# Optimization experiments

Measured on AMD Instinct MI355X. Metric: run time of the kernel, lower is better.

The kernel has to match this reference:

```python
import jax, jax.numpy as jnp
import numpy as np

N_NODES = 50000
N_EDGES = 800000
D = 128


def setup_inputs() -> dict:
    key = jax.random.key(0)
    ks = jax.random.split(key, 8)
    s = 1.0 / np.sqrt(D)
    return {
        "x": jax.random.normal(ks[0], (N_NODES, D), dtype=jnp.float32),
        "edge_index": jax.random.randint(ks[1], (2, N_EDGES), 0, N_NODES, dtype=jnp.int32),
        "W0l": jax.random.normal(ks[2], (D, D), dtype=jnp.float32) * s,
        "b0l": jnp.zeros((D,), dtype=jnp.float32),
        "W0r": jax.random.normal(ks[3], (D, D), dtype=jnp.float32) * s,
        "W1l": jax.random.normal(ks[4], (D, D), dtype=jnp.float32) * s,
        "b1l": jnp.zeros((D,), dtype=jnp.float32),
        "W1r": jax.random.normal(ks[5], (D, D), dtype=jnp.float32) * s,
    }


def reference(x, edge_index, W0l, b0l, W0r, W1l, b1l, W1r):
    # Encoder(conv='sage', num_layers=2), eval mode (dropout = identity).
    src = edge_index[0]  # x_j gathered from source nodes
    dst = edge_index[1]  # aggregated at target nodes
    # in-degree for mean aggregation; isolated nodes get 0 aggregate (PyG mean)
    deg = jax.ops.segment_sum(jnp.ones_like(dst, dtype=x.dtype), dst, num_segments=N_NODES)
    inv_deg = jnp.where(deg > 0, 1.0 / jnp.maximum(deg, 1.0), 0.0)[:, None]

    def sage(h, Wl, bl, Wr):
        m = h @ Wl + bl                                        # lin_l
        agg = jax.ops.segment_sum(m[src], dst, num_segments=N_NODES) * inv_deg  # mean aggr
        return agg + h @ Wr                                    # + lin_r skip

    h = jax.nn.relu(sage(x, W0l, b0l, W0r))   # layer 0 + relu
    return sage(h, W1l, b1l, W1r)             # final layer
```

## Files before the change

kernel.cpp:

```cpp
#include <hip/hip_runtime.h>

#define N_NODES 50000
#define N_EDGES 800000
#define D 128
#define CAP64 64
#define EIDXN (N_NODES * CAP64)

#define NSB 196
#define EPB 4096
#define NFB 1563
#define CCAP 20
#define SEDGE_CAP 768

typedef __bf16 bf16x8 __attribute__((ext_vector_type(8)));
typedef short s16x8 __attribute__((ext_vector_type(8)));
typedef float f32x4 __attribute__((ext_vector_type(4)));
typedef float f32x2 __attribute__((ext_vector_type(2)));
typedef unsigned short u16;
typedef unsigned int u32;
typedef unsigned char u8;
typedef u32 u32x2 __attribute__((ext_vector_type(2)));
typedef u32 u32x4 __attribute__((ext_vector_type(4)));
typedef u16 u16x4 __attribute__((ext_vector_type(4)));

__device__ inline u16 f32_to_bf16(float f) {
    u32 u = __builtin_bit_cast(u32, f);
    u += 0x7fffu + ((u >> 16) & 1u);
    return (u16)(u >> 16);
}

__device__ inline f32x4 mfma16(s16x8 a, s16x8 b, f32x4 c) {
    return __builtin_amdgcn_mfma_f32_16x16x32_bf16(
        __builtin_bit_cast(bf16x8, a), __builtin_bit_cast(bf16x8, b), c, 0, 0, 0);
}

#define CAST_BLOCKS ((N_NODES * 16) / 256)

__global__ __launch_bounds__(256) void prep_stage(
    const float* __restrict__ x, u16* __restrict__ xb,
    u8* __restrict__ xf8, u8* __restrict__ hf8,
    const float* __restrict__ W0l, const float* __restrict__ W0r,
    const float* __restrict__ W1l, const float* __restrict__ W1r,
    u16* __restrict__ Wp,
    const int* __restrict__ src, const int* __restrict__ dst,
    u32* __restrict__ staged, u8* __restrict__ ccnt) {
    __shared__ u32 cnt[NFB];
    int t = threadIdx.x, b = blockIdx.x;
    if (b < CAST_BLOCKS) {
        int gid = b * 256 + t;
        const float* p = x + (size_t)gid * 8;
        f32x4 a = *(const f32x4*)p;
        f32x4 c = *(const f32x4*)(p + 4);
        u16 o[8];
#pragma unroll
        for (int j = 0; j < 4; j++) { o[j] = f32_to_bf16(a[j]); o[4 + j] = f32_to_bf16(c[j]); }
        *(s16x8*)(xb + (size_t)gid * 8) = *(const s16x8*)o;
        int p0 = __builtin_amdgcn_cvt_pk_fp8_f32(a.x, a.y, 0, false);
        int p1 = __builtin_amdgcn_cvt_pk_fp8_f32(a.z, a.w, 0, false);
        int p2 = __builtin_amdgcn_cvt_pk_fp8_f32(c.x, c.y, 0, false);
        int p3 = __builtin_amdgcn_cvt_pk_fp8_f32(c.z, c.w, 0, false);
        u32x2 w;
        w.x = (u32)(p0 & 0xffff) | ((u32)(p1 & 0xffff) << 16);
        w.y = (u32)(p2 & 0xffff) | ((u32)(p3 & 0xffff) << 16);
        *(u32x2*)(xf8 + (size_t)gid * 8) = w;
    } else if (b < CAST_BLOCKS + 32) {
        int gid = (b - CAST_BLOCKS) * 256 + t;
        int wsel = gid >> 11;
        int rem  = gid & 2047;
        int ct   = rem >> 8;
        int ks   = (rem >> 6) & 3;
        int lane = rem & 63;
        const float* W = (wsel == 0) ? W0l : (wsel == 1) ? W0r : (wsel == 2) ? W1l : W1r;
        int n  = ct * 16 + (lane & 15);
        int k0 = ks * 32 + (lane >> 4) * 8;
        u16 o[8];
#pragma unroll
        for (int j = 0; j < 8; j++) o[j] = f32_to_bf16(W[(k0 + j) * D + n]);
        u16* dp = Wp + wsel * 16384 + (size_t)((ct * 4 + ks) * 64 + lane) * 8;
        *(s16x8*)dp = *(const s16x8*)o;
    } else if (b < CAST_BLOCKS + 33) {
        if (t < 32)       ((u32*)(xf8 + (size_t)N_NODES * D))[t] = 0;
        else if (t < 64)  ((u32*)(hf8 + (size_t)N_NODES * D))[t - 32] = 0;
    } else {
        int sb = b - CAST_BLOCKS - 33;
        for (int i = t; i < NFB; i += 256) cnt[i] = 0;
        __syncthreads();
        int bb = sb * EPB;
#pragma unroll
        for (int i = 0; i < 16; i++) {
            int e = bb + i * 256 + t;
            if (e < N_EDGES) {
                int sv = src[e], dv = dst[e];
                int fb = dv >> 5;
                u32 slot = atomicAdd(&cnt[fb], 1);
                if (slot < CCAP)
                    staged[((size_t)sb * NFB + fb) * CCAP + slot] =
                        (u32)sv | ((u32)(dv & 31) << 16);
            }
        }
        __syncthreads();
        for (int i = t; i < NFB; i += 256) {
            u32 c = cnt[i]; if (c > CCAP) c = CCAP;
            ccnt[(size_t)i * NSB + sb] = (u8)c;
        }
    }
}

__global__ __launch_bounds__(256) void fine_kernel(
    const u32* __restrict__ staged, const u8* __restrict__ ccnt,
    u16* __restrict__ eidx, int* __restrict__ cursor) {
    __shared__ u32 sedge[SEDGE_CAP];
    __shared__ u32 ncnt[32];
    __shared__ u32 total;
    int t = threadIdx.x, fb = blockIdx.x;
    if (t < 32) ncnt[t] = 0;
    if (t == 0) total = 0;
    __syncthreads();
    if (t < NSB) {
        u32 c = ccnt[(size_t)fb * NSB + t];
        if (c) {
            u32 base = atomicAdd(&total, c);
            const u32* sp = staged + ((size_t)t * NFB + fb) * CCAP;
            for (u32 j = 0; j < c; j++) {
                u32 bj = base + j;
                if (bj < SEDGE_CAP) sedge[bj] = sp[j];
            }
        }
    }
    __syncthreads();
    u32 tot = total; if (tot > SEDGE_CAP) tot = SEDGE_CAP;
    for (u32 i = t; i < tot; i += 256) {
        u32 v = sedge[i];
        u32 n32 = (v >> 16) & 31;
        u32 slot = atomicAdd(&ncnt[n32], 1);
        int node = (fb << 5) + (int)n32;
        if (slot < CAP64) eidx[((size_t)node << 6) + slot] = (u16)(v & 0xffffu);
    }
    __syncthreads();
    int node = (fb << 5) + t;
    if (t < 32 && node < N_NODES) {
        u32 dgc = ncnt[t]; if (dgc > CAP64) dgc = CAP64;
        cursor[node] = (int)dgc;
    }
}

__device__ inline void issue_e(u16x4 (&e)[2], const u16* __restrict__ eidx,
                               const int (&basek)[2], const int (&rnds)[2],
                               int quad, int rr) {
#pragma unroll
    for (int k = 0; k < 2; k++)
        if (rr < rnds[k]) e[k] = *(const u16x4*)(eidx + basek[k] + rr * 16 + quad * 4);
}
__device__ inline void issue_g(u32x2 (&g)[2][4], const u16x4 (&e)[2],
                               const u8* __restrict__ AF8, const int (&rnds)[2],
                               const int (&degk)[2], int quad, int ql, int rr) {
#pragma unroll
    for (int k = 0; k < 2; k++)
        if (rr < rnds[k]) {
            int sbase = rr * 16 + quad * 4;
#pragma unroll
            for (int j = 0; j < 4; j++) {
                int idx = (sbase + j < degk[k]) ? (int)e[k][j] : N_NODES;
                g[k][j] = *(const u32x2*)(AF8 + (size_t)idx * D + ql * 8);
            }
        }
}
__device__ inline void unpack_acc(f32x2 (&acc)[2][4], const u32x2 (&g)[2][4],
                                  const int (&rnds)[2], int rr) {
#pragma unroll
    for (int k = 0; k < 2; k++)
        if (rr < rnds[k]) {
#pragma unroll
            for (int j = 0; j < 4; j++) {
                u32x2 v = g[k][j];
                acc[k][0] += __builtin_amdgcn_cvt_pk_f32_fp8((int)v.x, false);
                acc[k][1] += __builtin_amdgcn_cvt_pk_f32_fp8((int)v.x, true);
                acc[k][2] += __builtin_amdgcn_cvt_pk_f32_fp8((int)v.y, false);
                acc[k][3] += __builtin_amdgcn_cvt_pk_f32_fp8((int)v.y, true);
            }
        }
}

template <int RELU, int OUTF32>
__global__ __launch_bounds__(512) void fused_layer(
    const u16* __restrict__ A, const u8* __restrict__ AF8,
    const u16* __restrict__ WpR, const u16* __restrict__ WpL,
    const float* __restrict__ bias, const int* __restrict__ cursor,
    const u16* __restrict__ eidx,
    u16* __restrict__ outb, u8* __restrict__ outf8, float* __restrict__ outf) {
    __shared__ char mlds[16 * 256];
    int wave = threadIdx.x >> 6, lane = threadIdx.x & 63;
    int rowbase = blockIdx.x * 16;
    int quad = lane >> 4, ql = lane & 15;

    int basek[2], rnds[2], degk[2];
#pragma unroll
    for (int k = 0; k < 2; k++) {
        int node = rowbase + wave * 2 + k;
        int dd = cursor[node];
        if (dd > CAP64) dd = CAP64;
        degk[k]  = dd;
        basek[k] = node << 6;
        rnds[k]  = (dd + 15) >> 4;
    }
    int maxr = rnds[0] > rnds[1] ? rnds[0] : rnds[1];

    f32x2 acc[2][4];
#pragma unroll
    for (int k = 0; k < 2; k++)
#pragma unroll
        for (int e = 0; e < 4; e++) acc[k][e] = (f32x2){0.f, 0.f};

    if (maxr > 0) {
        u16x4 eA[2], eB[2];
        u32x2 gA[2][4], gB[2][4];
        issue_e(eA, eidx, basek, rnds, quad, 0);
        issue_g(gA, eA, AF8, rnds, degk, quad, ql, 0);
        if (maxr > 1) issue_e(eB, eidx, basek, rnds, quad, 1);
        int r = 0;
        while (true) {
            if (r + 1 < maxr) issue_g(gB, eB, AF8, rnds, degk, quad, ql, r + 1);
            if (r + 2 < maxr) issue_e(eA, eidx, basek, rnds, quad, r + 2);
            unpack_acc(acc, gA, rnds, r);
            if (++r >= maxr) break;
            if (r + 1 < maxr) issue_g(gA, eA, AF8, rnds, degk, quad, ql, r + 1);
            if (r + 2 < maxr) issue_e(eB, eidx, basek, rnds, quad, r + 2);
            unpack_acc(acc, gB, rnds, r);
            if (++r >= maxr) break;
        }
    }

#pragma unroll
    for (int k = 0; k < 2; k++) {
        float v[8];
#pragma unroll
        for (int e = 0; e < 4; e++) { v[2 * e] = acc[k][e].x; v[2 * e + 1] = acc[k][e].y; }
#pragma unroll
        for (int j = 0; j < 8; j++) {
            v[j] += __shfl_xor(v[j], 16);
            v[j] += __shfl_xor(v[j], 32);
        }
        if (quad == 0) {
            float iv = degk[k] > 0 ? 1.0f / (float)degk[k] : 0.0f;
            u32x4 o;
            o.x = (u32)f32_to_bf16(v[0] * iv) | ((u32)f32_to_bf16(v[1] * iv) << 16);
            o.y = (u32)f32_to_bf16(v[2] * iv) | ((u32)f32_to_bf16(v[3] * iv) << 16);
            o.z = (u32)f32_to_bf16(v[4] * iv) | ((u32)f32_to_bf16(v[5] * iv) << 16);
            o.w = (u32)f32_to_bf16(v[6] * iv) | ((u32)f32_to_bf16(v[7] * iv) << 16);
            int lr = wave * 2 + k;
            *(u32x4*)(mlds + lr * 256 + ((ql ^ lr) & 15) * 16) = o;
        }
    }

    s16x8 bR[4], bL[4];
#pragma unroll
    for (int ks = 0; ks < 4; ks++) {
        size_t off = (size_t)((wave * 4 + ks) * 64 + lane) * 8;
        bR[ks] = *(const s16x8*)(WpR + off);
        bL[ks] = *(const s16x8*)(WpL + off);
    }
    __syncthreads();

    f32x4 acc2 = (f32x4){0.f, 0.f, 0.f, 0.f};
#pragma unroll
    for (int ks = 0; ks < 4; ks++) {
        s16x8 a1 = *(const s16x8*)(A + (size_t)(rowbase + ql) * D + ks * 32 + quad * 8);
        s16x8 a2 = *(const s16x8*)(mlds + ql * 256 + (((ks * 4 + quad) ^ ql) & 15) * 16);
        acc2 = mfma16(a1, bR[ks], acc2);
        acc2 = mfma16(a2, bL[ks], acc2);
    }

    float bv = bias[wave * 16 + ql];

#pragma unroll
    for (int i = 0; i < 4; i++) {
        int row = rowbase + quad * 4 + i;
        float mask = cursor[row] > 0 ? 1.f : 0.f;
        int col = wave * 16 + ql;
        float val = acc2[i] + mask * bv;
        if (RELU) val = val > 0.f ? val : 0.f;
        if (OUTF32) {
            outf[(size_t)row * D + col] = val;
        } else {
            outb[(size_t)row * D + col] = f32_to_bf16(val);
            int pk = __builtin_amdgcn_cvt_pk_fp8_f32(val, val, 0, false);
            outf8[(size_t)row * D + col] = (u8)(pk & 0xff);
        }
    }
}

extern "C" void kernel_launch(void* const* d_in, const int* in_sizes, int n_in,
                              void* d_out, int out_size, void* d_ws, size_t ws_size,
                              hipStream_t stream) {
    const float* x    = (const float*)d_in[0];
    const int*   edge = (const int*)d_in[1];
    const int*   src  = edge;
    const int*   dstn = edge + N_EDGES;
    const float* W0l  = (const float*)d_in[2];
    const float* b0l  = (const float*)d_in[3];
    const float* W0r  = (const float*)d_in[4];
    const float* W1l  = (const float*)d_in[5];
    const float* b1l  = (const float*)d_in[6];
    const float* W1r  = (const float*)d_in[7];
    float* out = (float*)d_out;

    char* p = (char*)d_ws;
    auto alloc = [&](size_t nb) { char* r = p; p += (nb + 255) & ~(size_t)255; return r; };
    int*   cursor = (int*)alloc((size_t)N_NODES * 4);
    u16*   eidx   = (u16*)alloc((size_t)EIDXN * 2);
    u16*   xb     = (u16*)alloc((size_t)N_NODES * D * 2);
    u16*   hb     = (u16*)alloc((size_t)N_NODES * D * 2);
    u8*    xf8    = (u8*)alloc((size_t)(N_NODES + 1) * D);
    u8*    hf8    = (u8*)alloc((size_t)(N_NODES + 1) * D);
    u16*   Wp     = (u16*)alloc((size_t)4 * 16384 * 2);
    u32*   staged = (u32*)alloc((size_t)NSB * NFB * CCAP * 4);
    u8*    ccnt   = (u8*)alloc((size_t)NFB * NSB);

    prep_stage<<<CAST_BLOCKS + 33 + NSB, 256, 0, stream>>>(
        x, xb, xf8, hf8, W0l, W0r, W1l, W1r, Wp, src, dstn, staged, ccnt);
    fine_kernel<<<NFB, 256, 0, stream>>>(staged, ccnt, eidx, cursor);

    int fblocks = N_NODES / 16;
    const u16* WpL0 = Wp;
    const u16* WpR0 = Wp + 16384;
    const u16* WpL1 = Wp + 2 * 16384;
    const u16* WpR1 = Wp + 3 * 16384;
    fused_layer<1, 0><<<fblocks, 512, 0, stream>>>(xb, xf8, WpR0, WpL0, b0l, cursor, eidx, hb, hf8, nullptr);
    fused_layer<0, 1><<<fblocks, 512, 0, stream>>>(hb, hf8, WpR1, WpL1, b1l, cursor, eidx, nullptr, nullptr, out);
}
```

Before: 210.1 us.

## Fuse prep, bucketing and both SAGE layers into one cooperative persistent kernel

Replaces the four launches (prep, fine bucketing, two fused layers) with a single cooperative kernel that uses grid.sync between phases. Bucketing now groups destinations by 16 instead of 32, matching the 16-row layer tile. The fine bucketing step and the layer-0 tile run in the same block, so layer 0 reads edge indices and degrees from LDS rather than global memory. The aim is to remove launch gaps and the eidx/cursor round trip for layer 0. In exchange the grid is capped by occupancy, so blocks loop over tiles, the grid barriers add cost, and the smaller per-bucket caps (CCAP 14, SEDGE_CAP 384) may drop edges for high-degree destination groups.

```diff
diff --git a/kernel.cpp b/kernel.cpp
--- a/kernel.cpp
+++ b/kernel.cpp
@@ -1,16 +1,21 @@
 #include <hip/hip_runtime.h>
+#include <hip/hip_cooperative_groups.h>
+
+namespace cg = cooperative_groups;
 
 #define N_NODES 50000
 #define N_EDGES 800000
 #define D 128
 #define CAP64 64
-#define EIDXN (N_NODES * CAP64)
-
+#define NBUCK 3125
 #define NSB 196
 #define EPB 4096
-#define NFB 1563
-#define CCAP 20
-#define SEDGE_CAP 768
+#define CCAP 14
+#define SEDGE_CAP 384
+
+#define CAST_UNITS 1563
+#define WU 16
+#define A_UNITS (CAST_UNITS + WU + 1 + NSB)
 
 typedef __bf16 bf16x8 __attribute__((ext_vector_type(8)));
 typedef short s16x8 __attribute__((ext_vector_type(8)));
@@ -34,126 +39,16 @@
         __builtin_bit_cast(bf16x8, a), __builtin_bit_cast(bf16x8, b), c, 0, 0, 0);
 }
 
-#define CAST_BLOCKS ((N_NODES * 16) / 256)
-
-__global__ __launch_bounds__(256) void prep_stage(
-    const float* __restrict__ x, u16* __restrict__ xb,
-    u8* __restrict__ xf8, u8* __restrict__ hf8,
-    const float* __restrict__ W0l, const float* __restrict__ W0r,
-    const float* __restrict__ W1l, const float* __restrict__ W1r,
-    u16* __restrict__ Wp,
-    const int* __restrict__ src, const int* __restrict__ dst,
-    u32* __restrict__ staged, u8* __restrict__ ccnt) {
-    __shared__ u32 cnt[NFB];
-    int t = threadIdx.x, b = blockIdx.x;
-    if (b < CAST_BLOCKS) {
-        int gid = b * 256 + t;
-        const float* p = x + (size_t)gid * 8;
-        f32x4 a = *(const f32x4*)p;
-        f32x4 c = *(const f32x4*)(p + 4);
-        u16 o[8];
-#pragma unroll
-        for (int j = 0; j < 4; j++) { o[j] = f32_to_bf16(a[j]); o[4 + j] = f32_to_bf16(c[j]); }
-        *(s16x8*)(xb + (size_t)gid * 8) = *(const s16x8*)o;
-        int p0 = __builtin_amdgcn_cvt_pk_fp8_f32(a.x, a.y, 0, false);
-        int p1 = __builtin_amdgcn_cvt_pk_fp8_f32(a.z, a.w, 0, false);
-        int p2 = __builtin_amdgcn_cvt_pk_fp8_f32(c.x, c.y, 0, false);
-        int p3 = __builtin_amdgcn_cvt_pk_fp8_f32(c.z, c.w, 0, false);
-        u32x2 w;
-        w.x = (u32)(p0 & 0xffff) | ((u32)(p1 & 0xffff) << 16);
-        w.y = (u32)(p2 & 0xffff) | ((u32)(p3 & 0xffff) << 16);
-        *(u32x2*)(xf8 + (size_t)gid * 8) = w;
-    } else if (b < CAST_BLOCKS + 32) {
-        int gid = (b - CAST_BLOCKS) * 256 + t;
-        int wsel = gid >> 11;
-        int rem  = gid & 2047;
-        int ct   = rem >> 8;
-        int ks   = (rem >> 6) & 3;
-        int lane = rem & 63;
-        const float* W = (wsel == 0) ? W0l : (wsel == 1) ? W0r : (wsel == 2) ? W1l : W1r;
-        int n  = ct * 16 + (lane & 15);
-        int k0 = ks * 32 + (lane >> 4) * 8;
-        u16 o[8];
-#pragma unroll
-        for (int j = 0; j < 8; j++) o[j] = f32_to_bf16(W[(k0 + j) * D + n]);
-        u16* dp = Wp + wsel * 16384 + (size_t)((ct * 4 + ks) * 64 + lane) * 8;
-        *(s16x8*)dp = *(const s16x8*)o;
-    } else if (b < CAST_BLOCKS + 33) {
-        if (t < 32)       ((u32*)(xf8 + (size_t)N_NODES * D))[t] = 0;
-        else if (t < 64)  ((u32*)(hf8 + (size_t)N_NODES * D))[t - 32] = 0;
-    } else {
-        int sb = b - CAST_BLOCKS - 33;
-        for (int i = t; i < NFB; i += 256) cnt[i] = 0;
-        __syncthreads();
-        int bb = sb * EPB;
-#pragma unroll
-        for (int i = 0; i < 16; i++) {
-            int e = bb + i * 256 + t;
-            if (e < N_EDGES) {
-                int sv = src[e], dv = dst[e];
-                int fb = dv >> 5;
-                u32 slot = atomicAdd(&cnt[fb], 1);
-                if (slot < CCAP)
-                    staged[((size_t)sb * NFB + fb) * CCAP + slot] =
-                        (u32)sv | ((u32)(dv & 31) << 16);
-            }
-        }
-        __syncthreads();
-        for (int i = t; i < NFB; i += 256) {
-            u32 c = cnt[i]; if (c > CCAP) c = CCAP;
-            ccnt[(size_t)i * NSB + sb] = (u8)c;
-        }
-    }
-}
-
-__global__ __launch_bounds__(256) void fine_kernel(
-    const u32* __restrict__ staged, const u8* __restrict__ ccnt,
-    u16* __restrict__ eidx, int* __restrict__ cursor) {
-    __shared__ u32 sedge[SEDGE_CAP];
-    __shared__ u32 ncnt[32];
-    __shared__ u32 total;
-    int t = threadIdx.x, fb = blockIdx.x;
-    if (t < 32) ncnt[t] = 0;
-    if (t == 0) total = 0;
-    __syncthreads();
-    if (t < NSB) {
-        u32 c = ccnt[(size_t)fb * NSB + t];
-        if (c) {
-            u32 base = atomicAdd(&total, c);
-            const u32* sp = staged + ((size_t)t * NFB + fb) * CCAP;
-            for (u32 j = 0; j < c; j++) {
-                u32 bj = base + j;
-                if (bj < SEDGE_CAP) sedge[bj] = sp[j];
-            }
-        }
-    }
-    __syncthreads();
-    u32 tot = total; if (tot > SEDGE_CAP) tot = SEDGE_CAP;
-    for (u32 i = t; i < tot; i += 256) {
-        u32 v = sedge[i];
-        u32 n32 = (v >> 16) & 31;
-        u32 slot = atomicAdd(&ncnt[n32], 1);
-        int node = (fb << 5) + (int)n32;
-        if (slot < CAP64) eidx[((size_t)node << 6) + slot] = (u16)(v & 0xffffu);
-    }
-    __syncthreads();
-    int node = (fb << 5) + t;
-    if (t < 32 && node < N_NODES) {
-        u32 dgc = ncnt[t]; if (dgc > CAP64) dgc = CAP64;
-        cursor[node] = (int)dgc;
-    }
-}
-
-__device__ inline void issue_e(u16x4 (&e)[2], const u16* __restrict__ eidx,
-                               const int (&basek)[2], const int (&rnds)[2],
-                               int quad, int rr) {
+__device__ __forceinline__ void issue_e(u16x4 (&e)[2], const u16* ebase,
+                                        const int (&basek)[2], const int (&rnds)[2],
+                                        int quad, int rr) {
 #pragma unroll
     for (int k = 0; k < 2; k++)
-        if (rr < rnds[k]) e[k] = *(const u16x4*)(eidx + basek[k] + rr * 16 + quad * 4);
-}
-__device__ inline void issue_g(u32x2 (&g)[2][4], const u16x4 (&e)[2],
-                               const u8* __restrict__ AF8, const int (&rnds)[2],
-                               const int (&degk)[2], int quad, int ql, int rr) {
+        if (rr < rnds[k]) e[k] = *(const u16x4*)(ebase + basek[k] + rr * 16 + quad * 4);
+}
+__device__ __forceinline__ void issue_g(u32x2 (&g)[2][4], const u16x4 (&e)[2],
+                                        const u8* __restrict__ AF8, const int (&rnds)[2],
+                                        const int (&degk)[2], int quad, int ql, int rr) {
 #pragma unroll
     for (int k = 0; k < 2; k++)
         if (rr < rnds[k]) {
@@ -165,8 +60,8 @@
             }
         }
 }
-__device__ inline void unpack_acc(f32x2 (&acc)[2][4], const u32x2 (&g)[2][4],
-                                  const int (&rnds)[2], int rr) {
+__device__ __forceinline__ void unpack_acc(f32x2 (&acc)[2][4], const u32x2 (&g)[2][4],
+                                           const int (&rnds)[2], int rr) {
 #pragma unroll
     for (int k = 0; k < 2; k++)
         if (rr < rnds[k]) {
@@ -181,26 +76,28 @@
         }
 }
 
-template <int RELU, int OUTF32>
-__global__ __launch_bounds__(512) void fused_layer(
+template <int RELU, int OUTF32, int LOCAL>
+__device__ __forceinline__ void sage_tile(
+    int fb, int t,
     const u16* __restrict__ A, const u8* __restrict__ AF8,
     const u16* __restrict__ WpR, const u16* __restrict__ WpL,
-    const float* __restrict__ bias, const int* __restrict__ cursor,
-    const u16* __restrict__ eidx,
+    const float* __restrict__ bias,
+    const int* __restrict__ cursor, const u16* __restrict__ eidx_g,
+    const u16* eidx_l, const u32* ncnt, char* mlds,
     u16* __restrict__ outb, u8* __restrict__ outf8, float* __restrict__ outf) {
-    __shared__ char mlds[16 * 256];
-    int wave = threadIdx.x >> 6, lane = threadIdx.x & 63;
-    int rowbase = blockIdx.x * 16;
+    int wave = t >> 6, lane = t & 63;
+    int rowbase = fb * 16;
     int quad = lane >> 4, ql = lane & 15;
+    const u16* ebase = LOCAL ? eidx_l : eidx_g;
 
     int basek[2], rnds[2], degk[2];
 #pragma unroll
     for (int k = 0; k < 2; k++) {
-        int node = rowbase + wave * 2 + k;
-        int dd = cursor[node];
+        int lr = wave * 2 + k;
+        int dd = LOCAL ? (int)ncnt[lr] : cursor[rowbase + lr];
         if (dd > CAP64) dd = CAP64;
         degk[k]  = dd;
-        basek[k] = node << 6;
+        basek[k] = LOCAL ? (lr << 6) : ((rowbase + lr) << 6);
         rnds[k]  = (dd + 15) >> 4;
     }
     int maxr = rnds[0] > rnds[1] ? rnds[0] : rnds[1];
@@ -214,17 +111,17 @@
     if (maxr > 0) {
         u16x4 eA[2], eB[2];
         u32x2 gA[2][4], gB[2][4];
-        issue_e(eA, eidx, basek, rnds, quad, 0);
+        issue_e(eA, ebase, basek, rnds, quad, 0);
         issue_g(gA, eA, AF8, rnds, degk, quad, ql, 0);
-        if (maxr > 1) issue_e(eB, eidx, basek, rnds, quad, 1);
+        if (maxr > 1) issue_e(eB, ebase, basek, rnds, quad, 1);
         int r = 0;
         while (true) {
             if (r + 1 < maxr) issue_g(gB, eB, AF8, rnds, degk, quad, ql, r + 1);
-            if (r + 2 < maxr) issue_e(eA, eidx, basek, rnds, quad, r + 2);
+            if (r + 2 < maxr) issue_e(eA, ebase, basek, rnds, quad, r + 2);
             unpack_acc(acc, gA, rnds, r);
             if (++r >= maxr) break;
             if (r + 1 < maxr) issue_g(gA, eA, AF8, rnds, degk, quad, ql, r + 1);
-            if (r + 2 < maxr) issue_e(eB, eidx, basek, rnds, quad, r + 2);
+            if (r + 2 < maxr) issue_e(eB, ebase, basek, rnds, quad, r + 2);
             unpack_acc(acc, gB, rnds, r);
             if (++r >= maxr) break;
         }
@@ -271,11 +168,11 @@
     }
 
     float bv = bias[wave * 16 + ql];
-
 #pragma unroll
     for (int i = 0; i < 4; i++) {
         int row = rowbase + quad * 4 + i;
-        float mask = cursor[row] > 0 ? 1.f : 0.f;
+        int dr = LOCAL ? (int)ncnt[quad * 4 + i] : cursor[row];
+        float mask = dr > 0 ? 1.f : 0.f;
         int col = wave * 16 + ql;
         float val = acc2[i] + mask * bv;
         if (RELU) val = val > 0.f ? val : 0.f;
@@ -286,6 +183,134 @@
             int pk = __builtin_amdgcn_cvt_pk_fp8_f32(val, val, 0, false);
             outf8[(size_t)row * D + col] = (u8)(pk & 0xff);
         }
+    }
+}
+
+__global__ __launch_bounds__(512, 8) void mega(
+    const float* __restrict__ x, const int* __restrict__ src, const int* __restrict__ dst,
+    const float* __restrict__ W0l, const float* __restrict__ b0l, const float* __restrict__ W0r,
+    const float* __restrict__ W1l, const float* __restrict__ b1l, const float* __restrict__ W1r,
+    u16* __restrict__ xb, u16* __restrict__ hb, u8* __restrict__ xf8, u8* __restrict__ hf8,
+    u16* __restrict__ Wp, u32* __restrict__ staged, u8* __restrict__ ccnt,
+    u16* __restrict__ eidx, int* __restrict__ cursor, float* __restrict__ out) {
+    cg::grid_group grid = cg::this_grid();
+    __shared__ u32 cnt[NBUCK];
+    __shared__ u32 sedge[SEDGE_CAP];
+    __shared__ u32 ncnt[16];
+    __shared__ u32 stotal;
+    __shared__ u16 eidx_l[16 * CAP64];
+    __shared__ char mlds[16 * 256];
+    int t = threadIdx.x;
+
+    const u16* WpL0 = Wp;
+    const u16* WpR0 = Wp + 16384;
+    const u16* WpL1 = Wp + 2 * 16384;
+    const u16* WpR1 = Wp + 3 * 16384;
+
+    for (int u = blockIdx.x; u < A_UNITS; u += gridDim.x) {
+        if (u < CAST_UNITS) {
+            int gid = u * 512 + t;
+            if (gid < N_NODES * 16) {
+                const float* p = x + (size_t)gid * 8;
+                f32x4 a = *(const f32x4*)p;
+                f32x4 c = *(const f32x4*)(p + 4);
+                u16 o[8];
+#pragma unroll
+                for (int j = 0; j < 4; j++) { o[j] = f32_to_bf16(a[j]); o[4 + j] = f32_to_bf16(c[j]); }
+                *(s16x8*)(xb + (size_t)gid * 8) = *(const s16x8*)o;
+                int p0 = __builtin_amdgcn_cvt_pk_fp8_f32(a.x, a.y, 0, false);
+                int p1 = __builtin_amdgcn_cvt_pk_fp8_f32(a.z, a.w, 0, false);
+                int p2 = __builtin_amdgcn_cvt_pk_fp8_f32(c.x, c.y, 0, false);
+                int p3 = __builtin_amdgcn_cvt_pk_fp8_f32(c.z, c.w, 0, false);
+                u32x2 w;
+                w.x = (u32)(p0 & 0xffff) | ((u32)(p1 & 0xffff) << 16);
+                w.y = (u32)(p2 & 0xffff) | ((u32)(p3 & 0xffff) << 16);
+                *(u32x2*)(xf8 + (size_t)gid * 8) = w;
+            }
+        } else if (u < CAST_UNITS + WU) {
+            int gid = (u - CAST_UNITS) * 512 + t;
+            int wsel = gid >> 11;
+            int rem  = gid & 2047;
+            int ct   = rem >> 8;
+            int ks   = (rem >> 6) & 3;
+            int lane = rem & 63;
+            const float* W = (wsel == 0) ? W0l : (wsel == 1) ? W0r : (wsel == 2) ? W1l : W1r;
+            int n  = ct * 16 + (lane & 15);
+            int k0 = ks * 32 + (lane >> 4) * 8;
+            u16 o[8];
+#pragma unroll
+            for (int j = 0; j < 8; j++) o[j] = f32_to_bf16(W[(k0 + j) * D + n]);
+            u16* dp = Wp + wsel * 16384 + (size_t)((ct * 4 + ks) * 64 + lane) * 8;
+            *(s16x8*)dp = *(const s16x8*)o;
+        } else if (u == CAST_UNITS + WU) {
+            if (t < 32)       ((u32*)(xf8 + (size_t)N_NODES * D))[t] = 0;
+            else if (t < 64)  ((u32*)(hf8 + (size_t)N_NODES * D))[t - 32] = 0;
+        } else {
+            int sb = u - (CAST_UNITS + WU + 1);
+            for (int i = t; i < NBUCK; i += 512) cnt[i] = 0;
+            __syncthreads();
+            int bb = sb * EPB;
+#pragma unroll
+            for (int i = 0; i < 8; i++) {
+                int e = bb + i * 512 + t;
+                if (e < N_EDGES) {
+                    int sv = src[e], dv = dst[e];
+                    int fb = dv >> 4;
+                    u32 slot = atomicAdd(&cnt[fb], 1);
+                    if (slot < CCAP)
+                        staged[((size_t)sb * NBUCK + fb) * CCAP + slot] =
+                            (u32)sv | ((u32)(dv & 15) << 16);
+                }
+            }
+            __syncthreads();
+            for (int i = t; i < NBUCK; i += 512) {
+                u32 c = cnt[i]; if (c > CCAP) c = CCAP;
+                ccnt[(size_t)i * NSB + sb] = (u8)c;
+            }
+            __syncthreads();
+        }
+    }
+    grid.sync();
+
+    for (int fb = blockIdx.x; fb < NBUCK; fb += gridDim.x) {
+        __syncthreads();
+        if (t < 16) ncnt[t] = 0;
+        if (t == 0) stotal = 0;
+        __syncthreads();
+        if (t < NSB) {
+            u32 c = ccnt[(size_t)fb * NSB + t];
+            if (c) {
+                u32 base = atomicAdd(&stotal, c);
+                const u32* sp = staged + ((size_t)t * NBUCK + fb) * CCAP;
+                for (u32 j = 0; j < c; j++) {
+                    u32 bj = base + j;
+                    if (bj < SEDGE_CAP) sedge[bj] = sp[j];
+                }
+            }
+        }
+        __syncthreads();
+        u32 tot = stotal; if (tot > SEDGE_CAP) tot = SEDGE_CAP;
+        for (u32 i = t; i < tot; i += 512) {
+            u32 v = sedge[i];
+            u32 n16 = (v >> 16) & 15;
+            u32 slot = atomicAdd(&ncnt[n16], 1);
+            if (slot < CAP64) eidx_l[(n16 << 6) + slot] = (u16)(v & 0xffffu);
+        }
+        __syncthreads();
+        ((u32*)eidx)[(size_t)fb * 512 + t] = ((const u32*)eidx_l)[t];
+        if (t < 16) {
+            u32 dgc = ncnt[t]; if (dgc > CAP64) dgc = CAP64;
+            cursor[fb * 16 + t] = (int)dgc;
+        }
+        sage_tile<1, 0, 1>(fb, t, xb, xf8, WpR0, WpL0, b0l,
+                           nullptr, nullptr, eidx_l, ncnt, mlds, hb, hf8, nullptr);
+    }
+    grid.sync();
+
+    for (int fb = blockIdx.x; fb < NBUCK; fb += gridDim.x) {
+        __syncthreads();
+        sage_tile<0, 1, 0>(fb, t, hb, hf8, WpR1, WpL1, b1l,
+                           cursor, eidx, nullptr, nullptr, mlds, nullptr, nullptr, out);
     }
 }
 
@@ -307,24 +332,30 @@
     char* p = (char*)d_ws;
     auto alloc = [&](size_t nb) { char* r = p; p += (nb + 255) & ~(size_t)255; return r; };
     int*   cursor = (int*)alloc((size_t)N_NODES * 4);
-    u16*   eidx   = (u16*)alloc((size_t)EIDXN * 2);
+    u16*   eidx   = (u16*)alloc((size_t)N_NODES * CAP64 * 2);
     u16*   xb     = (u16*)alloc((size_t)N_NODES * D * 2);
     u16*   hb     = (u16*)alloc((size_t)N_NODES * D * 2);
     u8*    xf8    = (u8*)alloc((size_t)(N_NODES + 1) * D);
     u8*    hf8    = (u8*)alloc((size_t)(N_NODES + 1) * D);
     u16*   Wp     = (u16*)alloc((size_t)4 * 16384 * 2);
-    u32*   staged = (u32*)alloc((size_t)NSB * NFB * CCAP * 4);
-    u8*    ccnt   = (u8*)alloc((size_t)NFB * NSB);
-
-    prep_stage<<<CAST_BLOCKS + 33 + NSB, 256, 0, stream>>>(
-        x, xb, xf8, hf8, W0l, W0r, W1l, W1r, Wp, src, dstn, staged, ccnt);
-    fine_kernel<<<NFB, 256, 0, stream>>>(staged, ccnt, eidx, cursor);
-
-    int fblocks = N_NODES / 16;
-    const u16* WpL0 = Wp;
-    const u16* WpR0 = Wp + 16384;
-    const u16* WpL1 = Wp + 2 * 16384;
-    const u16* WpR1 = Wp + 3 * 16384;
-    fused_layer<1, 0><<<fblocks, 512, 0, stream>>>(xb, xf8, WpR0, WpL0, b0l, cursor, eidx, hb, hf8, nullptr);
-    fused_layer<0, 1><<<fblocks, 512, 0, stream>>>(hb, hf8, WpR1, WpL1, b1l, cursor, eidx, nullptr, nullptr, out);
-}
+    u32*   staged = (u32*)alloc((size_t)NSB * NBUCK * CCAP * 4);
+    u8*    ccnt   = (u8*)alloc((size_t)NBUCK * NSB);
+
+    int mb = 0;
+    if (hipOccupancyMaxActiveBlocksPerMultiprocessor(
+            &mb, reinterpret_cast<const void*>(mega), 512, 0) != hipSuccess || mb < 1)
+        mb = 1;
+    long grid = (long)mb * 256;
+    if (grid > NBUCK) grid = NBUCK;
+
+    void* args[] = {
+        (void*)&x, (void*)&src, (void*)&dstn,
+        (void*)&W0l, (void*)&b0l, (void*)&W0r,
+        (void*)&W1l, (void*)&b1l, (void*)&W1r,
+        (void*)&xb, (void*)&hb, (void*)&xf8, (void*)&hf8,
+        (void*)&Wp, (void*)&staged, (void*)&ccnt,
+        (void*)&eidx, (void*)&cursor, (void*)&out
+    };
+    hipLaunchCooperativeKernel(reinterpret_cast<const void*>(mega),
+                               dim3((unsigned)grid), dim3(512), args, 0, stream);
+}
```

Measured after the change: 585.3 us. 2.79x slower.
